# Optimization experiments

Measured on AMD Instinct MI355X. Metric: run time of the kernel, lower is better.

## Reference

```python
import jax, jax.numpy as jnp
import numpy as np

ALPHA = 0.99   # config.alpha_grape
GAMMA = 0.999  # config.gamma
LAMBD = 0.7    # config.lambd_grape
T, A = 262144, 64


def setup_inputs() -> dict:
    key = jax.random.key(0)
    ks = jax.random.split(key, 7)
    q = jax.random.normal(ks[0], (T + 1, A), jnp.float32)
    q_tar = jax.random.normal(ks[1], (T + 1, A), jnp.float32)
    # pi / mu are probability distributions over actions (softmax of logits)
    pi = jax.nn.softmax(jax.random.normal(ks[2], (T + 1, A), jnp.float32), axis=-1)
    mu_t = jax.nn.softmax(jax.random.normal(ks[3], (T, A), jnp.float32), axis=-1)
    a_t = jax.random.randint(ks[4], (T,), 0, A, dtype=jnp.int32)
    r_t = jax.random.normal(ks[5], (T,), jnp.float32)
    done_t = jax.random.randint(ks[6], (T,), 0, 2, dtype=jnp.int32)
    return dict(q=q, q_tar=q_tar, pi=pi, a_t=a_t, r_t=r_t, mu_t=mu_t, done_t=done_t)


def reference(q, q_tar, pi, a_t, r_t, mu_t, done_t):
    # GRAPE.compute_targets
    l = q.shape[0] - 1
    idx = jnp.arange(l)
    pi_t, pi_tp1 = pi[:-1], pi[1:]
    q_t, q_tp1 = q[:-1], q_tar[1:]
    q_t_a = q_t[idx, a_t]                              # [T]
    v_t = jnp.sum(pi_t * q_t, axis=1)                  # [T]
    v_tp1 = jnp.sum(pi_tp1 * q_tp1, axis=1)            # [T]
    done_f = done_t.astype(q.dtype)
    q_t_a_est = r_t + (1.0 - done_f) * GAMMA * v_tp1
    td_error = q_t_a_est - q_t_a
    rho_t_a = pi_t[idx, a_t] / mu_t[idx, a_t]
    c_t_a = LAMBD * jnp.clip(rho_t_a, 0.0, 1.0)

    # backward-in-time first-order recurrence over y'
    def step(y_prime, xs):
        est, td, rho, c, d = xs
        y = jnp.where(d > 0.5, 0.0, y_prime)           # reset at episode end
        g = est + y
        y_new = LAMBD * GAMMA * rho * td + GAMMA * c * y
        return y_new, g

    _, g_q = jax.lax.scan(
        step, jnp.float32(0.0),
        (q_t_a_est, td_error, rho_t_a, c_t_a, done_f),
        reverse=True,
    )
    targets_q = g_q + ALPHA * (q_t_a - v_t)            # [T]
    advantages = (1.0 - ALPHA) * (q_t - v_t[:, None])  # [T, A]
    return targets_q, advantages
```

## Files before the change

### kernel.cpp

```cpp
#include <hip/hip_runtime.h>

#define GAMMA 0.999f
#define LAMBD 0.7f
#define ALPHA 0.99f

constexpr int A_DIM = 64;
constexpr int CH    = 128;
constexpr int BLK   = 256;

typedef float fx4 __attribute__((ext_vector_type(4)));

__device__ __forceinline__ float dot4(const float4& a, const float4& b) {
    return a.x*b.x + a.y*b.y + a.z*b.z + a.w*b.w;
}

__device__ __forceinline__ void nt_store4(float* p, float x, float y, float z, float w) {
    fx4 v = { x, y, z, w };
    __builtin_nontemporal_store(v, (fx4*)p);
}

__global__ __launch_bounds__(BLK, 4)
void k_main(const float* __restrict__ q, const float* __restrict__ q_tar,
            const float* __restrict__ pi, const int* __restrict__ a_t,
            const float* __restrict__ r_t, const float* __restrict__ mu_t,
            const int* __restrict__ done_t,
            float* __restrict__ adv_out,
            float2* __restrict__ comb, float2* __restrict__ cab)
{
    __shared__ float sQa[CH], sPa[CH], sMa[CH], sKm[CH], sRt[CH];
    __shared__ float sV[CH], sVp[CH];
    __shared__ float sWA[2], sWB[2];

    const int tid  = threadIdx.x;
    const int wave = tid >> 6, lane = tid & 63;
    const int sub  = lane >> 4, li = lane & 15;
    const int R0   = blockIdx.x * CH;

    if (tid < CH) {
        int r = R0 + tid;
        int a = a_t[r];
        sQa[tid] = q[r * A_DIM + a];
        sPa[tid] = pi[r * A_DIM + a];
    } else {
        int row = tid - CH;
        int r = R0 + row;
        int a = a_t[r];
        sMa[row] = mu_t[r * A_DIM + a];
        sRt[row] = r_t[r];
        sKm[row] = 1.0f - (float)done_t[r];
    }

    const int lrow0 = wave * 32 + sub;
    float4 piA, qA, pipA, qpA, piB, qB, pipB, qpB;
    {
        int gA = (R0 + lrow0) * A_DIM + li * 4;
        int gB = gA + 4 * A_DIM;
        piA  = *(const float4*)&pi[gA];
        qA   = *(const float4*)&q[gA];
        pipA = *(const float4*)&pi[gA + A_DIM];
        qpA  = *(const float4*)&q_tar[gA + A_DIM];
        piB  = *(const float4*)&pi[gB];
        qB   = *(const float4*)&q[gB];
        pipB = *(const float4*)&pi[gB + A_DIM];
        qpB  = *(const float4*)&q_tar[gB + A_DIM];
    }
    #pragma unroll
    for (int i = 0; i < 4; ++i) {
        float4 npiA, nqA, npipA, nqpA, npiB, nqB, npipB, nqpB;
        if (i < 3) {
            int gA = (R0 + lrow0 + (i + 1) * 8) * A_DIM + li * 4;
            int gB = gA + 4 * A_DIM;
            npiA  = *(const float4*)&pi[gA];
            nqA   = *(const float4*)&q[gA];
            npipA = *(const float4*)&pi[gA + A_DIM];
            nqpA  = *(const float4*)&q_tar[gA + A_DIM];
            npiB  = *(const float4*)&pi[gB];
            nqB   = *(const float4*)&q[gB];
            npipB = *(const float4*)&pi[gB + A_DIM];
            nqpB  = *(const float4*)&q_tar[gB + A_DIM];
        }

        int lrowA = lrow0 + i * 8;
        int lrowB = lrowA + 4;
        int gA = (R0 + lrowA) * A_DIM + li * 4;
        int gB = (R0 + lrowB) * A_DIM + li * 4;

        float s0A = dot4(piA, qA),  s1A = dot4(pipA, qpA);
        float s0B = dot4(piB, qB),  s1B = dot4(pipB, qpB);
        #pragma unroll
        for (int off = 1; off < 16; off <<= 1) {
            s0A += __shfl_xor(s0A, off);
            s1A += __shfl_xor(s1A, off);
            s0B += __shfl_xor(s0B, off);
            s1B += __shfl_xor(s1B, off);
        }

        nt_store4(&adv_out[gA],
                  (1.0f - ALPHA) * (qA.x - s0A), (1.0f - ALPHA) * (qA.y - s0A),
                  (1.0f - ALPHA) * (qA.z - s0A), (1.0f - ALPHA) * (qA.w - s0A));
        nt_store4(&adv_out[gB],
                  (1.0f - ALPHA) * (qB.x - s0B), (1.0f - ALPHA) * (qB.y - s0B),
                  (1.0f - ALPHA) * (qB.z - s0B), (1.0f - ALPHA) * (qB.w - s0B));

        if (li == 0) {
            sV[lrowA] = s0A;  sVp[lrowA] = s1A;
            sV[lrowB] = s0B;  sVp[lrowB] = s1B;
        }

        piA = npiA; qA = nqA; pipA = npipA; qpA = nqpA;
        piB = npiB; qB = nqB; pipB = npipB; qpB = nqpB;
    }
    __syncthreads();

    float Ai = 0.0f, Bi = 1.0f, Xa = 0.0f, Xb = 1.0f;
    float E = 0.0f, kmask = 0.0f;
    int   row = wave * 64 + lane;
    if (wave < 2) {
        float s0 = sV[row], s1 = sVp[row];
        kmask = sKm[row];
        float qa  = sQa[row];
        float rho = sPa[row] / sMa[row];
        float est = sRt[row] + kmask * (GAMMA * s1);
        float td  = est - qa;
        float c   = LAMBD * fminf(fmaxf(rho, 0.0f), 1.0f);
        float Fa  = (LAMBD * GAMMA) * rho * td;
        float Fb  = kmask * (GAMMA * c);
        E = est + ALPHA * (qa - s0);

        Ai = Fa; Bi = Fb;
        #pragma unroll
        for (int off = 1; off < 64; off <<= 1) {
            float An = __shfl_down(Ai, off);
            float Bn = __shfl_down(Bi, off);
            if (lane + off < 64) { Ai += Bi * An; Bi *= Bn; }
        }
        if (lane == 0) { sWA[wave] = Ai; sWB[wave] = Bi; }
        Xa = __shfl_down(Ai, 1);
        Xb = __shfl_down(Bi, 1);
        if (lane == 63) { Xa = 0.0f; Xb = 1.0f; }
    }
    __syncthreads();
    if (wave < 2) {
        if (wave == 0) {
            Xa = Xa + Xb * sWA[1];
            Xb = Xb * sWB[1];
        }
        comb[R0 + row] = make_float2(E + kmask * Xa, kmask * Xb);
        if (tid == 0)
            cab[blockIdx.x] = make_float2(Ai + Bi * sWA[1], Bi * sWB[1]);
    }
}

__global__ __launch_bounds__(BLK / 2, 8)
void k_fin(const float2* __restrict__ comb, const float2* __restrict__ cab,
           float* __restrict__ targets, int nch)
{
    __shared__ float sXa[128], sXb[128];
    __shared__ float sWA[2], sWB[2];
    __shared__ float sYe;
    const int tid = threadIdx.x, bid = blockIdx.x;
    const int wave = tid >> 6, lane = tid & 63;

    const float4* cab4 = (const float4*)cab;
    float A = 0.0f, B = 1.0f;
    #pragma unroll
    for (int j = 0; j < 8; ++j) {
        float4 u = cab4[tid * 8 + j];
        A += B * u.x; B *= u.y;
        A += B * u.z; B *= u.w;
    }

    float Ai = A, Bi = B;
    #pragma unroll
    for (int off = 1; off < 64; off <<= 1) {
        float An = __shfl_down(Ai, off);
        float Bn = __shfl_down(Bi, off);
        if (lane + off < 64) { Ai += Bi * An; Bi *= Bn; }
    }
    if (lane == 0) { sWA[wave] = Ai; sWB[wave] = Bi; }
    float Xa = __shfl_down(Ai, 1);
    float Xb = __shfl_down(Bi, 1);
    if (lane == 63) { Xa = 0.0f; Xb = 1.0f; }
    __syncthreads();
    if (wave == 0) {
        Xa = Xa + Xb * sWA[1];
        Xb = Xb * sWB[1];
    }
    sXa[tid] = Xa; sXb[tid] = Xb;
    __syncthreads();

    if (tid == 0) {
        int c1 = bid + 1;
        float ye;
        if (c1 >= nch) {
            ye = 0.0f;
        } else {
            int jq = c1 >> 4;
            float Aa = sXa[jq], Bb = sXb[jq];
            for (int k2 = 16 * jq + 15; k2 >= c1; --k2) {
                float2 cv = cab[k2];
                Aa = cv.x + cv.y * Aa;
                Bb = cv.y * Bb;
            }
            ye = Aa;
        }
        sYe = ye;
    }
    __syncthreads();

    float2 uw = comb[bid * CH + tid];
    __builtin_nontemporal_store(uw.x + uw.y * sYe, &targets[bid * CH + tid]);
}

extern "C" void kernel_launch(void* const* d_in, const int* in_sizes, int n_in,
                              void* d_out, int out_size, void* d_ws, size_t ws_size,
                              hipStream_t stream) {
    const float* q      = (const float*)d_in[0];
    const float* q_tar  = (const float*)d_in[1];
    const float* pi     = (const float*)d_in[2];
    const int*   a_t    = (const int*)  d_in[3];
    const float* r_t    = (const float*)d_in[4];
    const float* mu_t   = (const float*)d_in[5];
    const int*   done_t = (const int*)  d_in[6];

    const int T   = in_sizes[3];
    const int nch = T / CH;

    float* targets = (float*)d_out;
    float* adv     = (float*)d_out + T;

    char* ws = (char*)d_ws;
    float2* comb = (float2*)ws;              ws += (size_t)8 * T;
    float2* cab  = (float2*)ws;

    k_main<<<nch, BLK, 0, stream>>>(q, q_tar, pi, a_t, r_t, mu_t, done_t,
                                    adv, comb, cab);
    k_fin<<<nch, BLK / 2, 0, stream>>>(comb, cab, targets, nch);
}
```

Before: 63.29 us.

## Fuse two-kernel scan into single-pass decoupled look-back chained scan

Merges the main kernel and the finalize kernel into one launch that uses a decoupled look-back scan: each block publishes its chunk aggregate with a flag, then wave 0 looks back over predecessor flags and aggregates to get the carry-in. Blocks are processed in reverse order so the backward recurrence resolves in launch order. This removes the intermediate comb buffer round-trip and the second kernel launch, but adds a memset of the flags, spin-waiting on global atomics, and reliance on forward-progress ordering of block scheduling. Launch bounds are also raised to allow more resident blocks.

```diff
diff --git a/kernel.cpp b/kernel.cpp
--- a/kernel.cpp
+++ b/kernel.cpp
@@ -13,28 +13,38 @@
 __device__ __forceinline__ float dot4(const float4& a, const float4& b) {
     return a.x*b.x + a.y*b.y + a.z*b.z + a.w*b.w;
 }
-
 __device__ __forceinline__ void nt_store4(float* p, float x, float y, float z, float w) {
     fx4 v = { x, y, z, w };
     __builtin_nontemporal_store(v, (fx4*)p);
 }
-
-__global__ __launch_bounds__(BLK, 4)
+__device__ __forceinline__ unsigned long long pack2(float a, float b) {
+    union { float f[2]; unsigned long long u; } x;
+    x.f[0] = a; x.f[1] = b; return x.u;
+}
+__device__ __forceinline__ float2 unpack2(unsigned long long u) {
+    union { unsigned long long u; float f[2]; } x;
+    x.u = u; return make_float2(x.f[0], x.f[1]);
+}
+
+__global__ __launch_bounds__(BLK, 8)
 void k_main(const float* __restrict__ q, const float* __restrict__ q_tar,
             const float* __restrict__ pi, const int* __restrict__ a_t,
             const float* __restrict__ r_t, const float* __restrict__ mu_t,
             const int* __restrict__ done_t,
-            float* __restrict__ adv_out,
-            float2* __restrict__ comb, float2* __restrict__ cab)
+            float* __restrict__ adv_out, float* __restrict__ targets,
+            unsigned long long* __restrict__ st_ab,
+            unsigned long long* __restrict__ st_flag, int nch)
 {
     __shared__ float sQa[CH], sPa[CH], sMa[CH], sKm[CH], sRt[CH];
     __shared__ float sV[CH], sVp[CH];
     __shared__ float sWA[2], sWB[2];
+    __shared__ float sYe;
 
     const int tid  = threadIdx.x;
     const int wave = tid >> 6, lane = tid & 63;
     const int sub  = lane >> 4, li = lane & 15;
-    const int R0   = blockIdx.x * CH;
+    const int bid  = blockIdx.x;
+    const int R0   = (nch - 1 - bid) * CH;
 
     if (tid < CH) {
         int r = R0 + tid;
@@ -114,7 +124,7 @@
 
     float Ai = 0.0f, Bi = 1.0f, Xa = 0.0f, Xb = 1.0f;
     float E = 0.0f, kmask = 0.0f;
-    int   row = wave * 64 + lane;
+    const int row = wave * 64 + lane;
     if (wave < 2) {
         float s0 = sV[row], s1 = sVp[row];
         kmask = sKm[row];
@@ -140,76 +150,74 @@
         if (lane == 63) { Xa = 0.0f; Xb = 1.0f; }
     }
     __syncthreads();
-    if (wave < 2) {
-        if (wave == 0) {
-            Xa = Xa + Xb * sWA[1];
-            Xb = Xb * sWB[1];
-        }
-        comb[R0 + row] = make_float2(E + kmask * Xa, kmask * Xb);
-        if (tid == 0)
-            cab[blockIdx.x] = make_float2(Ai + Bi * sWA[1], Bi * sWB[1]);
-    }
-}
-
-__global__ __launch_bounds__(BLK / 2, 8)
-void k_fin(const float2* __restrict__ comb, const float2* __restrict__ cab,
-           float* __restrict__ targets, int nch)
-{
-    __shared__ float sXa[128], sXb[128];
-    __shared__ float sWA[2], sWB[2];
-    __shared__ float sYe;
-    const int tid = threadIdx.x, bid = blockIdx.x;
-    const int wave = tid >> 6, lane = tid & 63;
-
-    const float4* cab4 = (const float4*)cab;
-    float A = 0.0f, B = 1.0f;
-    #pragma unroll
-    for (int j = 0; j < 8; ++j) {
-        float4 u = cab4[tid * 8 + j];
-        A += B * u.x; B *= u.y;
-        A += B * u.z; B *= u.w;
-    }
-
-    float Ai = A, Bi = B;
-    #pragma unroll
-    for (int off = 1; off < 64; off <<= 1) {
-        float An = __shfl_down(Ai, off);
-        float Bn = __shfl_down(Bi, off);
-        if (lane + off < 64) { Ai += Bi * An; Bi *= Bn; }
-    }
-    if (lane == 0) { sWA[wave] = Ai; sWB[wave] = Bi; }
-    float Xa = __shfl_down(Ai, 1);
-    float Xb = __shfl_down(Bi, 1);
-    if (lane == 63) { Xa = 0.0f; Xb = 1.0f; }
-    __syncthreads();
+
+    float U = 0.0f, W = 0.0f;
+    float totA = 0.0f, totB = 1.0f;
     if (wave == 0) {
         Xa = Xa + Xb * sWA[1];
         Xb = Xb * sWB[1];
-    }
-    sXa[tid] = Xa; sXb[tid] = Xb;
+        totA = Ai + Bi * sWA[1];
+        totB = Bi * sWB[1];
+        if (lane == 0) {
+            __hip_atomic_store(&st_ab[bid], pack2(totA, totB),
+                               __ATOMIC_RELAXED, __HIP_MEMORY_SCOPE_AGENT);
+            __hip_atomic_store(&st_flag[bid], 1ull,
+                               __ATOMIC_RELEASE, __HIP_MEMORY_SCOPE_AGENT);
+        }
+    }
+    if (wave < 2) {
+        U = E + kmask * Xa;
+        W = kmask * Xb;
+    }
+
+    if (wave == 0) {
+        float Aa = 0.0f, Bb = 1.0f;
+        int base = bid - 1;
+        bool done = (base < 0);
+        while (!done) {
+            int n = (base + 1 < 64) ? base + 1 : 64;
+            int j = base - lane;
+            unsigned long long f = 1;
+            float2 v = make_float2(0.0f, 1.0f);
+            if (lane < n) {
+                do {
+                    f = __hip_atomic_load(&st_flag[j], __ATOMIC_ACQUIRE,
+                                          __HIP_MEMORY_SCOPE_AGENT);
+                    if (f == 0) __builtin_amdgcn_s_sleep(1);
+                } while (f == 0);
+                v = unpack2(__hip_atomic_load(&st_ab[j], __ATOMIC_RELAXED,
+                                              __HIP_MEMORY_SCOPE_AGENT));
+            }
+            unsigned long long bal = __ballot(lane < n && f == 2);
+            int L = bal ? (__ffsll((long long)bal) - 1) : (n - 1);
+            float Pa = v.x, Pb = v.y;
+            #pragma unroll
+            for (int off = 1; off < 64; off <<= 1) {
+                float Uu = __shfl_up(Pa, off);
+                float Vv = __shfl_up(Pb, off);
+                if (lane >= off) { Pa = Uu + Vv * Pa; Pb = Vv * Pb; }
+            }
+            float Wa = __shfl(Pa, L);
+            float Wb = __shfl(Pb, L);
+            Aa = Aa + Bb * Wa;
+            Bb = Bb * Wb;
+            done = (bal != 0) || (base - L - 1 < 0);
+            base -= (L + 1);
+        }
+        if (lane == 0) {
+            __hip_atomic_store(&st_ab[bid], pack2(totA + totB * Aa, totB * Bb),
+                               __ATOMIC_RELAXED, __HIP_MEMORY_SCOPE_AGENT);
+            __hip_atomic_store(&st_flag[bid], 2ull,
+                               __ATOMIC_RELEASE, __HIP_MEMORY_SCOPE_AGENT);
+            sYe = Aa;
+        }
+    }
     __syncthreads();
 
-    if (tid == 0) {
-        int c1 = bid + 1;
-        float ye;
-        if (c1 >= nch) {
-            ye = 0.0f;
-        } else {
-            int jq = c1 >> 4;
-            float Aa = sXa[jq], Bb = sXb[jq];
-            for (int k2 = 16 * jq + 15; k2 >= c1; --k2) {
-                float2 cv = cab[k2];
-                Aa = cv.x + cv.y * Aa;
-                Bb = cv.y * Bb;
-            }
-            ye = Aa;
-        }
-        sYe = ye;
-    }
-    __syncthreads();
-
-    float2 uw = comb[bid * CH + tid];
-    __builtin_nontemporal_store(uw.x + uw.y * sYe, &targets[bid * CH + tid]);
+    if (wave < 2) {
+        float ye = sYe;
+        __builtin_nontemporal_store(U + W * ye, &targets[R0 + row]);
+    }
 }
 
 extern "C" void kernel_launch(void* const* d_in, const int* in_sizes, int n_in,
@@ -230,10 +238,10 @@
     float* adv     = (float*)d_out + T;
 
     char* ws = (char*)d_ws;
-    float2* comb = (float2*)ws;              ws += (size_t)8 * T;
-    float2* cab  = (float2*)ws;
-
+    unsigned long long* st_ab   = (unsigned long long*)ws;
+    unsigned long long* st_flag = (unsigned long long*)(ws + (size_t)8 * nch);
+
+    hipMemsetAsync(st_flag, 0, (size_t)8 * nch, stream);
     k_main<<<nch, BLK, 0, stream>>>(q, q_tar, pi, a_t, r_t, mu_t, done_t,
-                                    adv, comb, cab);
-    k_fin<<<nch, BLK / 2, 0, stream>>>(comb, cab, targets, nch);
-}
+                                    adv, targets, st_ab, st_flag, nch);
+}
```

Measured after the change: 246.7 us. 3.9x slower.
